# Kernel tuning notes

Measured on AMD Instinct MI355X. Metric: run time of the kernel, lower is better.

Reference implementation:

```python
import jax, jax.numpy as jnp
import numpy as np

B, GL, GF, N = 4, 4, 128, 1024
CS, CN, NA = 32, 16, 16
S, HS = 512, 512


def squash(s, axis):
    # mag_sq/(1+mag_sq) * s/mag == s * mag/(1+mag_sq)
    mag_sq = jnp.sum(s * s, axis=axis, keepdims=True)
    return s * (jnp.sqrt(mag_sq) / (1.0 + mag_sq))


def routing(u_hat, n_iter=3):
    # u_hat: [M, I, J, U]; dynamic routing, softmax over J, squash over J (as in source)
    M, I, J, U = u_hat.shape
    b = jnp.zeros((I, J), dtype=u_hat.dtype)
    v = None
    for _ in range(n_iter):
        c = jax.nn.softmax(b, axis=1)                       # [I, J]
        s = jnp.einsum('ij,miju->mju', c, u_hat)            # [M, J, U]
        v = squash(s, axis=1)                               # squash over J (torch dim=2)
        b = b + jnp.einsum('miju,mju->mij', u_hat, v).mean(axis=0)
    return v


def setup_inputs():
    key = jax.random.key(0)
    ks = jax.random.split(key, 7)
    sc = 0.1
    return {
        'graph_embed': jax.random.normal(ks[0], (B, GL, GF, N), jnp.float32),
        'hidden': jax.random.normal(ks[1], (B, S, HS), jnp.float32),
        'Wp': jax.random.normal(ks[2], (GL, CS, GL, GF), jnp.float32) * sc,  # per-unit conv kernels
        'bp': jax.random.normal(ks[3], (GL, CS), jnp.float32) * sc,
        'Wg': jax.random.normal(ks[4], (CS, CN, CS, GL), jnp.float32) * sc,  # graph caps [I,J,U,K]
        'Wa': jax.random.normal(ks[5], (CS + HS,), jnp.float32) * sc,        # attention_1 weight
        'Ws': jax.random.normal(ks[6], (CN, NA, CS, CS), jnp.float32) * sc,  # aspect caps [I,J,U,K]
    }


def _per_example(x, h, Wp, bp, Wg, Wa, Ws):
    # x: [GL, GF, N], h: [S, HS]
    gl, gf, n = x.shape
    # primary capsules: each unit's conv kernel covers all (GL,GF) -> full contraction
    u = jnp.einsum('uclf,lfn->ucn', Wp, x) + bp[:, :, None]   # [GL, CS, N]
    u = squash(u.reshape(gl, -1), axis=1)                     # squash over CS*N (torch dim=2)
    p = u.reshape(n, gl, CS)                                  # torch .view(-1, GL, CS)
    # graph capsule routing
    u_hat_g = jnp.einsum('ijuk,mik->miju', Wg, p.transpose(0, 2, 1))  # [N, CS, CN, CS]
    v_g = routing(u_hat_g)                                    # [N, CN, CS]
    g = v_g.reshape(n, CS, CN).mean(axis=0).reshape(CN, CS)   # torch .view semantics
    # adaptive attention: Linear([g;h]) with no bias, softmax over capsules
    score = jax.nn.softmax((g @ Wa[:CS])[None, :] + (h @ Wa[CS:])[:, None], axis=1)  # [S, CN]
    condensed = g[None, :, :] * score[:, :, None]             # [S, CN, CS]
    # aspect capsule routing (transpose(1,2) then layer-internal transpose cancel out)
    u_hat_a = jnp.einsum('ijuk,mik->miju', Ws, condensed)     # [S, CN, NA, CS]
    return routing(u_hat_a)                                   # [S, NA, CS]


def reference(graph_embed, hidden, Wp, bp, Wg, Wa, Ws):
    f = jax.vmap(_per_example, in_axes=(0, 0, None, None, None, None, None))
    return f(graph_embed, hidden, Wp, bp, Wg, Wa, Ws)   # [B, S, NA, CS]
```

## Files before the change

### kernel.cpp

```cpp
#include <hip/hip_runtime.h>
#include <math.h>


static constexpr int OFF_U  = 0;
static constexpr int OFF_S  = 524288;
static constexpr int OFF_SS = 2621440;
static constexpr int OFF_BG = 2621456;
static constexpr int OFF_G  = 2623504;
static constexpr int OFF_UH = 2625552;

__global__ void k_primary_part(const float* __restrict__ X, const float* __restrict__ Wp,
                               float* __restrict__ ws)
{
    __shared__ float Wt[128 * 68];
    float* Upart = ws + OFF_S;
    if (blockIdx.x == 0 && blockIdx.y == 0 && blockIdx.z == 0) {
        float* Z = ws + OFF_SS;
        for (int i = threadIdx.x; i < 4112; i += 256) Z[i] = 0.f;
    }
    const int ct = blockIdx.x, nt = blockIdx.y;
    const int b = blockIdx.z >> 2, ks = blockIdx.z & 3;
    const int t = threadIdx.x;
    const int tn = t & 15, tc = t >> 4;
    const int c0 = ct * 64, n0 = nt * 64;
#pragma unroll
    for (int i = 0; i < 8; ++i) {
        const int idx = t + i * 256;
        const int c = idx >> 5, k4 = idx & 31;
        const float4 wv = *(const float4*)&Wp[(size_t)(c0 + c) * 512 + ks * 128 + k4 * 4];
        Wt[(k4 * 4 + 0) * 68 + c] = wv.x;
        Wt[(k4 * 4 + 1) * 68 + c] = wv.y;
        Wt[(k4 * 4 + 2) * 68 + c] = wv.z;
        Wt[(k4 * 4 + 3) * 68 + c] = wv.w;
    }
    __syncthreads();
    float acc[4][4] = {};
    const float* Xp = X + (size_t)b * 524288 + (size_t)(ks * 128) * 1024 + n0 + tn * 4;
#pragma unroll 4
    for (int k = 0; k < 128; ++k) {
        const float4 xv = *(const float4*)(Xp + (size_t)k * 1024);
        const float4 wv = *(const float4*)&Wt[k * 68 + tc * 4];
        const float w[4] = {wv.x, wv.y, wv.z, wv.w};
        const float x[4] = {xv.x, xv.y, xv.z, xv.w};
#pragma unroll
        for (int ci = 0; ci < 4; ++ci)
#pragma unroll
            for (int ni = 0; ni < 4; ++ni)
                acc[ci][ni] = fmaf(w[ci], x[ni], acc[ci][ni]);
    }
    float* up = Upart + (size_t)ks * 524288 + (size_t)b * 131072;
#pragma unroll
    for (int ci = 0; ci < 4; ++ci)
        *(float4*)&up[(size_t)(c0 + tc * 4 + ci) * 1024 + n0 + tn * 4] =
            make_float4(acc[ci][0], acc[ci][1], acc[ci][2], acc[ci][3]);
}

__global__ void k_reduceU(const float* __restrict__ bp, float* __restrict__ ws)
{
    __shared__ float red[256];
    const float* Upart = ws + OFF_S;
    float* U  = ws + OFF_U;
    float* SS = ws + OFF_SS;
    const int blk = blockIdx.x, t = threadIdx.x;
    const int b = blk >> 5, cg = blk & 31;
    float ssq = 0.f;
#pragma unroll
    for (int i = 0; i < 4; ++i) {
        const int c = cg * 4 + i;
        const int f4 = b * 32768 + c * 256 + t;
        float4 s = ((const float4*)Upart)[f4];
#pragma unroll
        for (int ks = 1; ks < 4; ++ks) {
            const float4 p = ((const float4*)Upart)[ks * 131072 + f4];
            s.x += p.x; s.y += p.y; s.z += p.z; s.w += p.w;
        }
        const float bv = bp[c];
        s.x += bv; s.y += bv; s.z += bv; s.w += bv;
        ssq = fmaf(s.x, s.x, ssq); ssq = fmaf(s.y, s.y, ssq);
        ssq = fmaf(s.z, s.z, ssq); ssq = fmaf(s.w, s.w, ssq);
        ((float4*)U)[f4] = s;
    }
    red[t] = ssq;
    __syncthreads();
    for (int s = 128; s > 0; s >>= 1) {
        if (t < s) red[t] += red[t + s];
        __syncthreads();
    }
    if (t == 0) atomicAdd(&SS[b * 4 + (cg >> 3)], red[0]);
}

__global__ void k_smatmul(const float* __restrict__ Wg, float* __restrict__ ws)
{
    __shared__ float Pt[64 * 65];
    __shared__ float Ct[64 * 65];
    __shared__ float cls[512];
    const float* U  = ws + OFF_U;
    const float* SS = ws + OFF_SS;
    const float* Bg = ws + OFF_BG;
    float* S = ws + OFF_S;
    const int mt = blockIdx.x, jt = blockIdx.y, b = blockIdx.z;
    const int t = threadIdx.x;
    const int tj = t & 15, tm = t >> 4;
    if (t < 32) {
        float vals[16];
        float mx = -1e30f;
        for (int j = 0; j < 16; ++j) { vals[j] = Bg[b * 512 + t * 16 + j]; mx = fmaxf(mx, vals[j]); }
        float sum = 0.f;
        for (int j = 0; j < 16; ++j) { vals[j] = expf(vals[j] - mx); sum += vals[j]; }
        const float inv = 1.f / sum;
        for (int j = 0; j < 16; ++j) cls[t * 16 + j] = vals[j] * inv;
    }
    const float ssv = SS[b * 4 + (mt >> 2)];
    const float sc = sqrtf(ssv) / (1.f + ssv);
    float acc[4][4] = {};
    const float* Ub = U + (size_t)b * 131072 + (size_t)mt * 64 * 128;
    __syncthreads();
    for (int kc = 0; kc < 2; ++kc) {
        for (int x = t; x < 64 * 64; x += 256) {
            const int r = x >> 6, cq = x & 63;
            Pt[r * 65 + cq] = Ub[r * 128 + kc * 64 + cq] * sc;
            const int q = kc * 64 + cq;
            const int i = q & 31, kk = q >> 5;
            const int ju = jt * 64 + r;
            const int j = ju >> 5, uu = ju & 31;
            Ct[r * 65 + cq] = cls[i * 16 + j] * Wg[((i * 16 + j) * 32 + uu) * 4 + kk];
        }
        __syncthreads();
        for (int q = 0; q < 64; ++q) {
            float pv[4], cv[4];
#pragma unroll
            for (int mm = 0; mm < 4; ++mm) pv[mm] = Pt[(tm * 4 + mm) * 65 + q];
#pragma unroll
            for (int jj = 0; jj < 4; ++jj) cv[jj] = Ct[(tj * 4 + jj) * 65 + q];
#pragma unroll
            for (int mm = 0; mm < 4; ++mm)
#pragma unroll
                for (int jj = 0; jj < 4; ++jj)
                    acc[mm][jj] = fmaf(pv[mm], cv[jj], acc[mm][jj]);
        }
        __syncthreads();
    }
#pragma unroll
    for (int mm = 0; mm < 4; ++mm) {
        float4 w = make_float4(acc[mm][0], acc[mm][1], acc[mm][2], acc[mm][3]);
        *(float4*)(S + (size_t)b * 524288 + (size_t)(mt * 64 + tm * 4 + mm) * 512
                     + jt * 64 + tj * 4) = w;
    }
}

__global__ void k_tbu(const float* __restrict__ Wg, float* __restrict__ ws)
{
    __shared__ float Ps[64 * 132];
    __shared__ float Vs[64 * 68];
    __shared__ float msS[64 * 32];
    __shared__ float bup[64];
    const float* U  = ws + OFF_U;
    const float* SS = ws + OFF_SS;
    const float* S  = ws + OFF_S;
    float* Bg = ws + OFF_BG;
    const int jt = blockIdx.x, mc = blockIdx.y, b = blockIdx.z;
    const int t = threadIdx.x;
    const int tq = t & 31, tjv = t >> 5;
    const int m0 = mc * 64;
    if (t < 64) bup[t] = 0.f;
    {
        const int uu = t & 31, rg = t >> 5;
#pragma unroll
        for (int mi = 0; mi < 8; ++mi) {
            const int r = rg * 8 + mi;
            const float* row = S + (size_t)b * 524288 + (size_t)(m0 + r) * 512;
            float mag = 0.f;
#pragma unroll
            for (int j = 0; j < 16; ++j) { const float v = row[j * 32 + uu]; mag = fmaf(v, v, mag); }
            msS[r * 32 + uu] = sqrtf(mag) / (1.f + mag);
        }
    }
    const float ssv = SS[b * 4 + (mc >> 2)];
    const float sc = sqrtf(ssv) / (1.f + ssv);
    __syncthreads();
#pragma unroll
    for (int i = 0; i < 8; ++i) {
        const int f4 = t + i * 256;
        const int r = f4 >> 5, q4 = f4 & 31;
        float4 v = *(const float4*)&U[(size_t)b * 131072 + (size_t)(m0 + r) * 128 + q4 * 4];
        v.x *= sc; v.y *= sc; v.z *= sc; v.w *= sc;
        *(float4*)&Ps[r * 132 + q4 * 4] = v;
    }
#pragma unroll
    for (int i = 0; i < 4; ++i) {
        const int f4 = t + i * 256;
        const int r = f4 >> 4, c4 = f4 & 15;
        const int m = m0 + r;
        float4 v = *(const float4*)&S[(size_t)b * 524288 + (size_t)m * 512 + jt * 64 + c4 * 4];
        const int ub = (c4 * 4) & 31;
        v.x *= msS[r * 32 + ub + 0]; v.y *= msS[r * 32 + ub + 1];
        v.z *= msS[r * 32 + ub + 2]; v.w *= msS[r * 32 + ub + 3];
        *(float4*)&Vs[r * 68 + c4 * 4] = v;
    }
    __syncthreads();
    float acc[4][8] = {};
#pragma unroll 2
    for (int m = 0; m < 64; ++m) {
        const float4 p4 = *(const float4*)&Ps[m * 132 + tq * 4];
        const float4 va = *(const float4*)&Vs[m * 68 + tjv * 8];
        const float4 vb = *(const float4*)&Vs[m * 68 + tjv * 8 + 4];
        const float pv[4] = {p4.x, p4.y, p4.z, p4.w};
        const float vv[8] = {va.x, va.y, va.z, va.w, vb.x, vb.y, vb.z, vb.w};
#pragma unroll
        for (int qi = 0; qi < 4; ++qi)
#pragma unroll
            for (int ji = 0; ji < 8; ++ji)
                acc[qi][ji] = fmaf(pv[qi], vv[ji], acc[qi][ji]);
    }
    const int k = tq >> 3;
    const int j_loc = tjv >> 2;
    const int j = jt * 2 + j_loc;
    const int u0 = (tjv & 3) * 8;
#pragma unroll
    for (int qi = 0; qi < 4; ++qi) {
        const int i = (tq & 7) * 4 + qi;
        const float* wp = Wg + ((i * 16 + j) * 32) * 4 + k;
        float s = 0.f;
#pragma unroll
        for (int ji = 0; ji < 8; ++ji)
            s = fmaf(wp[(u0 + ji) * 4], acc[qi][ji], s);
        s += __shfl_xor(s, 8);
        s += __shfl_xor(s, 16);
        s += __shfl_xor(s, 32);
        if ((t & 56) == 0) atomicAdd(&bup[i * 2 + j_loc], s);
    }
    __syncthreads();
    if (t < 64) {
        const int ii = t >> 1, jl = t & 1;
        atomicAdd(&Bg[b * 512 + ii * 16 + jt * 2 + jl], bup[t] * (1.f / 1024.f));
    }
}

__global__ void k_maggmean(float* __restrict__ ws)
{
    __shared__ float gacc[512];
    const float* S = ws + OFF_S;
    float* G = ws + OFF_G;
    const int t = threadIdx.x;
    gacc[t] = 0.f; gacc[t + 256] = 0.f;
    const int uu = t & 31, mlg = t >> 5;
    const int b = blockIdx.y;
    const int m0 = blockIdx.x * 32 + mlg * 4;
    float preg[16];
#pragma unroll
    for (int j = 0; j < 16; ++j) preg[j] = 0.f;
    __syncthreads();
#pragma unroll
    for (int mi = 0; mi < 4; ++mi) {
        const float* row = S + (size_t)b * 524288 + (size_t)(m0 + mi) * 512;
        float sv[16];
        float mag = 0.f;
#pragma unroll
        for (int j = 0; j < 16; ++j) { sv[j] = row[j * 32 + uu]; mag = fmaf(sv[j], sv[j], mag); }
        const float msc = sqrtf(mag) / (1.f + mag);
#pragma unroll
        for (int j = 0; j < 16; ++j) preg[j] = fmaf(sv[j], msc, preg[j]);
    }
#pragma unroll
    for (int j = 0; j < 16; ++j) atomicAdd(&gacc[j * 32 + uu], preg[j]);
    __syncthreads();
    atomicAdd(&G[b * 512 + t], gacc[t] * (1.f / 1024.f));
    atomicAdd(&G[b * 512 + 256 + t], gacc[t + 256] * (1.f / 1024.f));
}

__global__ void k_uhat(const float* __restrict__ Wa, const float* __restrict__ Wsp,
                       float* __restrict__ ws)
{
    const float* G = ws + OFF_G;
    float* UH = ws + OFF_UH;
    const int b = blockIdx.y;
    const int t = threadIdx.x;
    __shared__ float g[512], cond[512], score[16], red[16];
    g[t] = G[b * 512 + t];
    g[t + 256] = G[b * 512 + 256 + t];
    __syncthreads();
    if (t < 16) {
        float s = 0.f;
        for (int uu = 0; uu < 32; ++uu) s = fmaf(g[t * 32 + uu], Wa[uu], s);
        red[t] = s;
    }
    __syncthreads();
    if (t == 0) {
        float mx = -1e30f;
        for (int j = 0; j < 16; ++j) mx = fmaxf(mx, red[j]);
        float sum = 0.f;
        for (int j = 0; j < 16; ++j) { score[j] = expf(red[j] - mx); sum += score[j]; }
        const float inv = 1.f / sum;
        for (int j = 0; j < 16; ++j) score[j] *= inv;
    }
    __syncthreads();
    cond[t] = g[t] * score[t >> 5];
    cond[t + 256] = g[t + 256] * score[(t + 256) >> 5];
    __syncthreads();
    const int e0 = blockIdx.x * 1024 + t * 4;
    const int i = e0 >> 9;
    const float* cp = cond + i * 32;
    const float* wp = Wsp + (size_t)e0 * 32;
    float res[4];
#pragma unroll
    for (int jj = 0; jj < 4; ++jj) {
        float s = 0.f;
#pragma unroll
        for (int k8 = 0; k8 < 8; ++k8) {
            const float4 w = *(const float4*)(wp + jj * 32 + k8 * 4);
            s = fmaf(w.x, cp[k8 * 4 + 0], s);
            s = fmaf(w.y, cp[k8 * 4 + 1], s);
            s = fmaf(w.z, cp[k8 * 4 + 2], s);
            s = fmaf(w.w, cp[k8 * 4 + 3], s);
        }
        res[jj] = s;
    }
    ((float4*)UH)[(b * 8192 + e0) >> 2] = make_float4(res[0], res[1], res[2], res[3]);
}

__global__ void k_route_out(float* __restrict__ ws, float* __restrict__ out)
{
    const float* UH = ws + OFF_UH;
    const int bid = blockIdx.x;
    const int t = threadIdx.x;
    __shared__ float uh[8192], ba[256], cc[256], sbuf[512], msc[32];
    const int b = bid >> 6;
#pragma unroll
    for (int i = 0; i < 8; ++i)
        ((float4*)uh)[i * 256 + t] = ((const float4*)UH)[b * 2048 + i * 256 + t];
    ba[t] = 0.f;
    __syncthreads();
    for (int it = 0; it < 3; ++it) {
        if (t < 16) {
            float mx = -1e30f;
            for (int j = 0; j < 16; ++j) mx = fmaxf(mx, ba[t * 16 + j]);
            float sum = 0.f;
            for (int j = 0; j < 16; ++j) { cc[t * 16 + j] = expf(ba[t * 16 + j] - mx); sum += cc[t * 16 + j]; }
            const float inv = 1.f / sum;
            for (int j = 0; j < 16; ++j) cc[t * 16 + j] *= inv;
        }
        __syncthreads();
        for (int h = 0; h < 2; ++h) {
            const int e = h * 256 + t;
            const int j = e >> 5;
            float s = 0.f;
            for (int i = 0; i < 16; ++i) s = fmaf(cc[i * 16 + j], uh[i * 512 + e], s);
            sbuf[e] = s;
        }
        __syncthreads();
        if (t < 32) {
            float mg = 0.f;
            for (int j = 0; j < 16; ++j) { const float x = sbuf[j * 32 + t]; mg = fmaf(x, x, mg); }
            msc[t] = sqrtf(mg) / (1.f + mg);
        }
        __syncthreads();
        for (int h = 0; h < 2; ++h) {
            const int e = h * 256 + t;
            sbuf[e] *= msc[e & 31];
        }
        __syncthreads();
        if (it < 2) {
            const int i = t >> 4, j = t & 15;
            float s = 0.f;
            for (int uu = 0; uu < 32; ++uu) s = fmaf(uh[i * 512 + j * 32 + uu], sbuf[j * 32 + uu], s);
            ba[t] += s;
            __syncthreads();
        }
    }
#pragma unroll
    for (int i = 0; i < 4; ++i) {
        const int idx = bid * 1024 + i * 256 + t;
        const int jv4 = idx & 127;
        ((float4*)out)[idx] = *(const float4*)&sbuf[jv4 * 4];
    }
}

extern "C" void kernel_launch(void* const* d_in, const int* in_sizes, int n_in,
                              void* d_out, int out_size, void* d_ws, size_t ws_size,
                              hipStream_t stream)
{
    const float* X   = (const float*)d_in[0];
    const float* Wp  = (const float*)d_in[2];
    const float* bp  = (const float*)d_in[3];
    const float* Wg  = (const float*)d_in[4];
    const float* Wa  = (const float*)d_in[5];
    const float* Wsp = (const float*)d_in[6];
    float* out = (float*)d_out;
    float* ws  = (float*)d_ws;

    k_primary_part<<<dim3(2, 16, 16), 256, 0, stream>>>(X, Wp, ws);
    k_reduceU<<<128, 256, 0, stream>>>(bp, ws);

    for (int it = 0; it < 3; ++it) {
        k_smatmul<<<dim3(16, 8, 4), 256, 0, stream>>>(Wg, ws);
        if (it < 2) k_tbu<<<dim3(8, 16, 4), 256, 0, stream>>>(Wg, ws);
        else        k_maggmean<<<dim3(32, 4), 256, 0, stream>>>(ws);
    }

    k_uhat<<<dim3(8, 4), 256, 0, stream>>>(Wa, Wsp, ws);
    k_route_out<<<256, 256, 0, stream>>>(ws, out);
}
```

Before: 231.6 us.

## Fuse u_hat computation into routing kernel, vectorize smatmul tiles, widen reduceU grid

The aspect u_hat kernel is folded into k_route_out, so each block recomputes the batch's 8192-element u_hat in shared memory. This removes one launch and the workspace round trip, but every block now redoes the 4-way shared computation: 64 blocks per batch each read all of Ws. k_smatmul switches to float4 global loads and float4 LDS reads with a padded row stride of 68. k_reduceU runs twice as many blocks, each handling half as many channels.

```diff
diff --git a/kernel.cpp b/kernel.cpp
--- a/kernel.cpp
+++ b/kernel.cpp
@@ -7,7 +7,6 @@
 static constexpr int OFF_SS = 2621440;
 static constexpr int OFF_BG = 2621456;
 static constexpr int OFF_G  = 2623504;
-static constexpr int OFF_UH = 2625552;
 
 __global__ void k_primary_part(const float* __restrict__ X, const float* __restrict__ Wp,
                                float* __restrict__ ws)
@@ -62,11 +61,11 @@
     float* U  = ws + OFF_U;
     float* SS = ws + OFF_SS;
     const int blk = blockIdx.x, t = threadIdx.x;
-    const int b = blk >> 5, cg = blk & 31;
+    const int b = blk >> 6, cg = blk & 63;
     float ssq = 0.f;
 #pragma unroll
-    for (int i = 0; i < 4; ++i) {
-        const int c = cg * 4 + i;
+    for (int i = 0; i < 2; ++i) {
+        const int c = cg * 2 + i;
         const int f4 = b * 32768 + c * 256 + t;
         float4 s = ((const float4*)Upart)[f4];
 #pragma unroll
@@ -86,13 +85,13 @@
         if (t < s) red[t] += red[t + s];
         __syncthreads();
     }
-    if (t == 0) atomicAdd(&SS[b * 4 + (cg >> 3)], red[0]);
+    if (t == 0) atomicAdd(&SS[b * 4 + (cg >> 4)], red[0]);
 }
 
 __global__ void k_smatmul(const float* __restrict__ Wg, float* __restrict__ ws)
 {
-    __shared__ float Pt[64 * 65];
-    __shared__ float Ct[64 * 65];
+    __shared__ float Pt[64 * 68];
+    __shared__ float Ct[64 * 68];
     __shared__ float cls[512];
     const float* U  = ws + OFF_U;
     const float* SS = ws + OFF_SS;
@@ -116,27 +115,39 @@
     const float* Ub = U + (size_t)b * 131072 + (size_t)mt * 64 * 128;
     __syncthreads();
     for (int kc = 0; kc < 2; ++kc) {
-        for (int x = t; x < 64 * 64; x += 256) {
+#pragma unroll
+        for (int x = t; x < 1024; x += 256) {
+            const int r = x >> 4, c4 = x & 15;
+            float4 v = *(const float4*)&Ub[r * 128 + kc * 64 + c4 * 4];
+            v.x *= sc; v.y *= sc; v.z *= sc; v.w *= sc;
+            *(float4*)&Pt[r * 68 + c4 * 4] = v;
+        }
+#pragma unroll
+        for (int x = t; x < 4096; x += 256) {
             const int r = x >> 6, cq = x & 63;
-            Pt[r * 65 + cq] = Ub[r * 128 + kc * 64 + cq] * sc;
             const int q = kc * 64 + cq;
             const int i = q & 31, kk = q >> 5;
             const int ju = jt * 64 + r;
             const int j = ju >> 5, uu = ju & 31;
-            Ct[r * 65 + cq] = cls[i * 16 + j] * Wg[((i * 16 + j) * 32 + uu) * 4 + kk];
-        }
-        __syncthreads();
-        for (int q = 0; q < 64; ++q) {
-            float pv[4], cv[4];
-#pragma unroll
-            for (int mm = 0; mm < 4; ++mm) pv[mm] = Pt[(tm * 4 + mm) * 65 + q];
-#pragma unroll
-            for (int jj = 0; jj < 4; ++jj) cv[jj] = Ct[(tj * 4 + jj) * 65 + q];
+            Ct[r * 68 + cq] = cls[i * 16 + j] * Wg[((i * 16 + j) * 32 + uu) * 4 + kk];
+        }
+        __syncthreads();
+#pragma unroll 4
+        for (int q4 = 0; q4 < 16; ++q4) {
+            float4 pv[4], cv[4];
+#pragma unroll
+            for (int mm = 0; mm < 4; ++mm) pv[mm] = *(const float4*)&Pt[(tm * 4 + mm) * 68 + q4 * 4];
+#pragma unroll
+            for (int jj = 0; jj < 4; ++jj) cv[jj] = *(const float4*)&Ct[(tj * 4 + jj) * 68 + q4 * 4];
 #pragma unroll
             for (int mm = 0; mm < 4; ++mm)
 #pragma unroll
-                for (int jj = 0; jj < 4; ++jj)
-                    acc[mm][jj] = fmaf(pv[mm], cv[jj], acc[mm][jj]);
+                for (int jj = 0; jj < 4; ++jj) {
+                    acc[mm][jj] = fmaf(pv[mm].x, cv[jj].x, acc[mm][jj]);
+                    acc[mm][jj] = fmaf(pv[mm].y, cv[jj].y, acc[mm][jj]);
+                    acc[mm][jj] = fmaf(pv[mm].z, cv[jj].z, acc[mm][jj]);
+                    acc[mm][jj] = fmaf(pv[mm].w, cv[jj].w, acc[mm][jj]);
+                }
         }
         __syncthreads();
     }
@@ -268,16 +279,18 @@
     atomicAdd(&G[b * 512 + 256 + t], gacc[t + 256] * (1.f / 1024.f));
 }
 
-__global__ void k_uhat(const float* __restrict__ Wa, const float* __restrict__ Wsp,
-                       float* __restrict__ ws)
+__global__ void k_route_out(const float* __restrict__ Wa, const float* __restrict__ Wsp,
+                            float* __restrict__ ws, float* __restrict__ out)
 {
     const float* G = ws + OFF_G;
-    float* UH = ws + OFF_UH;
-    const int b = blockIdx.y;
-    const int t = threadIdx.x;
-    __shared__ float g[512], cond[512], score[16], red[16];
+    const int bid = blockIdx.x;
+    const int t = threadIdx.x;
+    __shared__ float uh[8192], g[512], cond[512], ba[256], cc[256], sbuf[512];
+    __shared__ float msc[32], score[16], red[16];
+    const int b = bid >> 6;
     g[t] = G[b * 512 + t];
     g[t + 256] = G[b * 512 + 256 + t];
+    ba[t] = 0.f;
     __syncthreads();
     if (t < 16) {
         float s = 0.f;
@@ -297,38 +310,23 @@
     cond[t] = g[t] * score[t >> 5];
     cond[t + 256] = g[t + 256] * score[(t + 256) >> 5];
     __syncthreads();
-    const int e0 = blockIdx.x * 1024 + t * 4;
-    const int i = e0 >> 9;
-    const float* cp = cond + i * 32;
-    const float* wp = Wsp + (size_t)e0 * 32;
-    float res[4];
-#pragma unroll
-    for (int jj = 0; jj < 4; ++jj) {
+#pragma unroll 2
+    for (int r = 0; r < 32; ++r) {
+        const int e = r * 256 + t;
+        const int i = e >> 9;
+        const float* cp = cond + i * 32;
+        const float* wr = Wsp + (size_t)e * 32;
         float s = 0.f;
 #pragma unroll
         for (int k8 = 0; k8 < 8; ++k8) {
-            const float4 w = *(const float4*)(wp + jj * 32 + k8 * 4);
+            const float4 w = *(const float4*)(wr + k8 * 4);
             s = fmaf(w.x, cp[k8 * 4 + 0], s);
             s = fmaf(w.y, cp[k8 * 4 + 1], s);
             s = fmaf(w.z, cp[k8 * 4 + 2], s);
             s = fmaf(w.w, cp[k8 * 4 + 3], s);
         }
-        res[jj] = s;
-    }
-    ((float4*)UH)[(b * 8192 + e0) >> 2] = make_float4(res[0], res[1], res[2], res[3]);
-}
-
-__global__ void k_route_out(float* __restrict__ ws, float* __restrict__ out)
-{
-    const float* UH = ws + OFF_UH;
-    const int bid = blockIdx.x;
-    const int t = threadIdx.x;
-    __shared__ float uh[8192], ba[256], cc[256], sbuf[512], msc[32];
-    const int b = bid >> 6;
-#pragma unroll
-    for (int i = 0; i < 8; ++i)
-        ((float4*)uh)[i * 256 + t] = ((const float4*)UH)[b * 2048 + i * 256 + t];
-    ba[t] = 0.f;
+        uh[e] = s;
+    }
     __syncthreads();
     for (int it = 0; it < 3; ++it) {
         if (t < 16) {
@@ -389,7 +387,7 @@
     float* ws  = (float*)d_ws;
 
     k_primary_part<<<dim3(2, 16, 16), 256, 0, stream>>>(X, Wp, ws);
-    k_reduceU<<<128, 256, 0, stream>>>(bp, ws);
+    k_reduceU<<<256, 256, 0, stream>>>(bp, ws);
 
     for (int it = 0; it < 3; ++it) {
         k_smatmul<<<dim3(16, 8, 4), 256, 0, stream>>>(Wg, ws);
@@ -397,6 +395,5 @@
         else        k_maggmean<<<dim3(32, 4), 256, 0, stream>>>(ws);
     }
 
-    k_uhat<<<dim3(8, 4), 256, 0, stream>>>(Wa, Wsp, ws);
-    k_route_out<<<256, 256, 0, stream>>>(ws, out);
-}
+    k_route_out<<<256, 256, 0, stream>>>(Wa, Wsp, ws, out);
+}
```

Result: slower. 291.8 us (+26.0%).
